# Kernel optimization log

Measured on AMD Instinct MI355X. Metric: run time of the kernel, lower is better.

The kernel has to match this reference:

```python
import jax, jax.numpy as jnp
import numpy as np

N_HEAD, D_HEAD, D_MODEL, D_INNER, KSIZE = 16, 64, 1024, 4096, 3
LN_EPS = 1e-3  # keras LayerNormalization default epsilon


def _layernorm(x, g, b):
    m = jnp.mean(x, axis=-1, keepdims=True)
    v = jnp.var(x, axis=-1, keepdims=True)
    return (x - m) * jax.lax.rsqrt(v + LN_EPS) * g + b


def _conv1d_same(x, w, b):
    # x: [B, S, Cin], w: [K, Cin, Cout] (keras Conv1D layout)
    y = jax.lax.conv_general_dilated(x, w, window_strides=(1,), padding='SAME',
                                     dimension_numbers=('NWC', 'WIO', 'NWC'))
    return y + b


def setup_inputs() -> dict:
    key = jax.random.key(0)
    ks = jax.random.split(key, 12)
    B, S, D = 4, 1024, D_MODEL
    dec_inp = jax.random.normal(ks[0], (B, S, D), dtype=jnp.float32)
    # padding mask: True = valid token; ensure >=1 padded position per row
    lengths = jax.random.randint(ks[1], (B,), S // 2, S)
    mask = (jnp.arange(S)[None, :] < lengths[:, None])[:, :, None]  # [B,S,1] bool
    sd = 0.02
    qkv_w = jax.random.normal(ks[2], (D, 3 * N_HEAD * D_HEAD), dtype=jnp.float32) * sd
    qkv_b = jnp.zeros((3 * N_HEAD * D_HEAD,), dtype=jnp.float32)
    o_w = jax.random.normal(ks[3], (N_HEAD * D_HEAD, D), dtype=jnp.float32) * sd
    ln1_g = jnp.ones((D,), dtype=jnp.float32)
    ln1_b = jnp.zeros((D,), dtype=jnp.float32)
    conv1_w = jax.random.normal(ks[4], (KSIZE, D, D_INNER), dtype=jnp.float32) * sd
    conv1_b = jnp.zeros((D_INNER,), dtype=jnp.float32)
    conv2_w = jax.random.normal(ks[5], (KSIZE, D_INNER, D), dtype=jnp.float32) * sd
    conv2_b = jnp.zeros((D,), dtype=jnp.float32)
    ln2_g = jnp.ones((D,), dtype=jnp.float32)
    ln2_b = jnp.zeros((D,), dtype=jnp.float32)
    return dict(dec_inp=dec_inp, mask=mask, qkv_w=qkv_w, qkv_b=qkv_b, o_w=o_w,
                ln1_g=ln1_g, ln1_b=ln1_b, conv1_w=conv1_w, conv1_b=conv1_b,
                conv2_w=conv2_w, conv2_b=conv2_b, ln2_g=ln2_g, ln2_b=ln2_b)


def _forward(dec_inp, mask, qkv_w, qkv_b, o_w, ln1_g, ln1_b,
             conv1_w, conv1_b, conv2_w, conv2_b, ln2_g, ln2_b):
    B, S, D = dec_inp.shape
    H, dh = N_HEAD, D_HEAD
    scale = 1.0 / (dh ** 0.5)
    # --- MultiHeadAttn (post-lnorm; dropout inactive at inference) ---
    residual = dec_inp
    qkv = dec_inp @ qkv_w + qkv_b                       # [B,S,3*H*dh]
    hq, hk, hv = jnp.split(qkv, 3, axis=2)
    to_flat = lambda h: h.reshape(B, S, H, dh).transpose(0, 2, 1, 3).reshape(B * H, S, dh)
    q, k, v = to_flat(hq), to_flat(hk), to_flat(hv)
    score = jnp.einsum('bqd,bkd->bqk', q, k) * scale    # [B*H, S, S]
    # attn_mask = ~mask.squeeze(2): True at PAD positions (faithful to TF port)
    am = (~mask[:, :, 0]).astype(score.dtype)[:, None, :]    # [B,1,S]
    am = jnp.tile(am, (H, S, 1))                             # [B*H,S,S] (tile over batch axis, as in tf.tile)
    add = jnp.where(am.astype(bool), am, -jnp.inf)           # pad -> +1.0, valid -> -inf (as written in source)
    score = score + add
    prob = jax.nn.softmax(score, axis=2)
    vec = prob @ v                                      # [B*H,S,dh]
    # faithful to source reshapes: [B*H,S,dh] -> [H,B,S,dh] -> [B,S,H*dh]
    vec = vec.reshape(H, B, S, dh).transpose(1, 2, 0, 3).reshape(B, S, H * dh)
    attn_out = vec @ o_w
    out = _layernorm(residual + attn_out, ln1_g, ln1_b)
    # mask-multiply between blocks
    out = out * mask.astype(out.dtype)
    # --- PositionwiseConvFF (post-lnorm) ---
    core = _conv1d_same(out, conv1_w, conv1_b)
    core = jax.nn.relu(core)
    core = _conv1d_same(core, conv2_w, conv2_b)
    out = _layernorm(out + core, ln2_g, ln2_b)
    out = out * mask.astype(out.dtype)
    return out


def reference(dec_inp, mask, qkv_w, qkv_b, o_w, ln1_g, ln1_b,
              conv1_w, conv1_b, conv2_w, conv2_b, ln2_g, ln2_b):
    return _forward(dec_inp, mask, qkv_w, qkv_b, o_w, ln1_g, ln1_b,
                    conv1_w, conv1_b, conv2_w, conv2_b, ln2_g, ln2_b)
```

## Files before the change

kernel.cpp:

```cpp
#include <hip/hip_runtime.h>
#include <cstdint>
#include <cstddef>

typedef float f32x4 __attribute__((ext_vector_type(4)));
typedef __bf16 bf16x8 __attribute__((ext_vector_type(8)));
typedef unsigned short u16;

__device__ __forceinline__ float bf2f(u16 u) {
  union { unsigned int i; float f; } x; x.i = ((unsigned int)u) << 16; return x.f;
}
__device__ __forceinline__ u16 f2bf(float f) {
  union { float f; unsigned int i; } x; x.f = f;
  unsigned int i = x.i;
  i += 0x7fffu + ((i >> 16) & 1u);
  return (u16)(i >> 16);
}

#if defined(__has_builtin)
#if __has_builtin(__builtin_amdgcn_global_load_lds)
#define HAS_GLL 1
#endif
#endif

__device__ __forceinline__ void async16(const u16* g, u16* l) {
#ifdef HAS_GLL
  __builtin_amdgcn_global_load_lds((const __attribute__((address_space(1))) void*)(const void*)g,
                                   (__attribute__((address_space(3))) void*)(void*)l, 16, 0, 0);
#else
  *(uint4*)l = *(const uint4*)g;
#endif
}

__global__ void compact_mask(const unsigned char* __restrict__ mask,
                             int* __restrict__ padIdx, int* __restrict__ padCnt,
                             float* __restrict__ maskf) {
  const int b = blockIdx.x;
  const int lane = threadIdx.x;
  int stride = 1;
  if (mask[1] == 0) stride = (mask[4] != 0) ? 4 : 8;
  int cnt = 0;
  for (int s0 = 0; s0 < 1024; s0 += 64) {
    const int s = s0 + lane;
    const bool valid = (mask[(size_t)((b << 10) + s) * stride] != 0);
    maskf[(b << 10) + s] = valid ? 1.f : 0.f;
    const bool pad = !valid;
    const unsigned long long bal = __ballot(pad);
    const int rank = (int)__popcll(bal & ((1ull << lane) - 1ull));
    if (pad) padIdx[(b << 10) + cnt + rank] = s;
    cnt += (int)__popcll(bal);
  }
  if (lane == 0) padCnt[b] = cnt;
}

__global__ __launch_bounds__(256)
void f32_to_bf16(const float* __restrict__ in, u16* __restrict__ out, int n4) {
  const int i = blockIdx.x * 256 + threadIdx.x;
  if (i < n4) {
    const float4 v = ((const float4*)in)[i];
    u16 o[4] = { f2bf(v.x), f2bf(v.y), f2bf(v.z), f2bf(v.w) };
    ((ushort4*)out)[i] = *(const ushort4*)o;
  }
}

__global__ __launch_bounds__(256)
void transpose_f32_bf16(const float* __restrict__ in, u16* __restrict__ out, int R, int C) {
  __shared__ u16 tile[64][65];
  const int r0 = blockIdx.y << 6, c0 = blockIdx.x << 6;
  const int tid = threadIdx.x;
  const int lr = tid >> 3, lc = (tid & 7) << 3;
#pragma unroll
  for (int p = 0; p < 2; ++p) {
    const int row = lr + (p << 5);
    const float4 a = *(const float4*)(in + (size_t)(r0 + row) * C + c0 + lc);
    const float4 bq = *(const float4*)(in + (size_t)(r0 + row) * C + c0 + lc + 4);
    tile[row][lc + 0] = f2bf(a.x); tile[row][lc + 1] = f2bf(a.y);
    tile[row][lc + 2] = f2bf(a.z); tile[row][lc + 3] = f2bf(a.w);
    tile[row][lc + 4] = f2bf(bq.x); tile[row][lc + 5] = f2bf(bq.y);
    tile[row][lc + 6] = f2bf(bq.z); tile[row][lc + 7] = f2bf(bq.w);
  }
  __syncthreads();
#pragma unroll
  for (int p = 0; p < 2; ++p) {
    const int oc = lr + (p << 5);
    u16 tmp[8];
#pragma unroll
    for (int e = 0; e < 8; ++e) tmp[e] = tile[lc + e][oc];
    *(uint4*)(out + (size_t)(c0 + oc) * R + r0 + lc) = *(const uint4*)tmp;
  }
}

template<int NTAPS, bool RELU, int SPLITK, int KORIG, int NBN>
__global__ __launch_bounds__(256)
void gemm_bt(const u16* __restrict__ A, const u16* __restrict__ BT,
             const float* __restrict__ bias, u16* __restrict__ C, u16* __restrict__ Calt,
             int M, int N, const u16* __restrict__ zp) {
  __shared__ __align__(16) u16 As[128 * 64];
  __shared__ __align__(16) u16 Bs[128 * 64];
  const int tid = threadIdx.x;
  const int id = blockIdx.x + NBN * blockIdx.y;
  const int bm = ((id / (16 * NBN)) << 4) + (id & 15);
  const int bn = (id % (16 * NBN)) >> 4;
  const int m0 = bm << 7;
  const int n0 = bn << 7;
  const int kz = (SPLITK > 1) ? blockIdx.z : 0;
  constexpr int Ktot = NTAPS * KORIG;
  constexpr int kchunk = Ktot / SPLITK;
  const int lane = tid & 63;
  const int w = tid >> 6;
  const int wm = (w >> 1) << 6;
  const int wn = (w & 1) << 6;
  const int fr = lane & 15;
  const int quad = lane >> 4;
  const int srow = tid >> 3;
  const int scol = (tid & 7) << 3;
  const int sx = (((tid & 7) ^ (srow & 7)) << 3);

  f32x4 acc[4][4] = {};

  const int kbeg = kz * kchunk, kend = kbeg + kchunk;
  int k = kbeg;
  while (k < kend) {
    const int t = (NTAPS == 3) ? (k / KORIG) : 0;
    const int seg_end = (NTAPS == 3) ? min(kend, (t + 1) * KORIG) : kend;
    const int c0 = k - t * KORIG;
    const u16* aptr[4];
    const u16* bptr[4];
#pragma unroll
    for (int i = 0; i < 4; ++i) {
      const int row = srow + (i << 5);
      if (NTAPS == 3) {
        const int m = m0 + row;
        const int sp = (m & 1023) + t - 1;
        aptr[i] = ((unsigned)sp < 1024u) ? (A + (size_t)(m + t - 1) * KORIG + c0 + sx)
                                         : (zp + ((tid & 255) << 3));
      } else {
        aptr[i] = A + (size_t)(m0 + row) * KORIG + k + sx;
      }
      bptr[i] = BT + (size_t)(n0 + row) * Ktot + k + sx;
    }
    for (; k < seg_end; k += 64) {
#pragma unroll
      for (int i = 0; i < 4; ++i) {
        const int row = srow + (i << 5);
        async16(aptr[i], &As[(row << 6) + scol]);
        async16(bptr[i], &Bs[(row << 6) + scol]);
        aptr[i] += 64; bptr[i] += 64;
      }
      asm volatile("s_waitcnt vmcnt(0)" ::: "memory");
      __syncthreads();
#pragma unroll
      for (int ks = 0; ks < 64; ks += 32) {
        const int ccol = ((((ks >> 3) + quad) ^ (fr & 7)) << 3);
        bf16x8 af[4], bfr[4];
#pragma unroll
        for (int mi = 0; mi < 4; ++mi)
          af[mi] = *(const bf16x8*)&As[((wm + (mi << 4) + fr) << 6) + ccol];
#pragma unroll
        for (int ni = 0; ni < 4; ++ni)
          bfr[ni] = *(const bf16x8*)&Bs[((wn + (ni << 4) + fr) << 6) + ccol];
#pragma unroll
        for (int mi = 0; mi < 4; ++mi)
#pragma unroll
          for (int ni = 0; ni < 4; ++ni)
            acc[mi][ni] = __builtin_amdgcn_mfma_f32_16x16x32_bf16(af[mi], bfr[ni], acc[mi][ni], 0, 0, 0);
      }
      __syncthreads();
    }
  }
  const int rbase = m0 + wm + (quad << 2);
  const int cbase = n0 + wn + fr;
  u16* dst = C;
  if (SPLITK > 1 && kz > 0) dst = Calt + (size_t)(kz - 1) * ((size_t)M * N);
#pragma unroll
  for (int ni = 0; ni < 4; ++ni) {
    const int col = cbase + (ni << 4);
    const float bv = (SPLITK == 1 && bias) ? bias[col] : 0.f;
#pragma unroll
    for (int mi = 0; mi < 4; ++mi) {
#pragma unroll
      for (int r = 0; r < 4; ++r) {
        float v = acc[mi][ni][r] + bv;
        if (RELU) v = fmaxf(v, 0.f);
        dst[(size_t)(rbase + (mi << 4) + r) * N + col] = f2bf(v);
      }
    }
  }
}

#define BAR8() do { asm volatile("" ::: "memory"); __builtin_amdgcn_s_barrier(); asm volatile("" ::: "memory"); } while (0)
#define WAITV(N) asm volatile("s_waitcnt vmcnt(" #N ")" ::: "memory")

#define READ_A(SLOT) \
  _Pragma("unroll") for (int mi = 0; mi < 4; ++mi) \
  _Pragma("unroll") for (int ks = 0; ks < 2; ++ks) \
    af[mi][ks] = *(const bf16x8*)&As[SLOT][((wm + (mi << 4) + fr) << 6) + ((((ks << 2) + quad) ^ (fr & 7)) << 3)];
#define READ_B(SLOT, BFR) \
  _Pragma("unroll") for (int ni = 0; ni < 2; ++ni) \
  _Pragma("unroll") for (int ks = 0; ks < 2; ++ks) \
    BFR[ni][ks] = *(const bf16x8*)&Bs[SLOT][((wn + (ni << 4) + fr) << 6) + ((((ks << 2) + quad) ^ (fr & 7)) << 3)];
#define MFMA_PH(MH, NH, BFR) \
  __builtin_amdgcn_s_setprio(1); \
  _Pragma("unroll") for (int mi = 0; mi < 4; ++mi) \
  _Pragma("unroll") for (int ni = 0; ni < 2; ++ni) \
  _Pragma("unroll") for (int ks = 0; ks < 2; ++ks) \
    acc[MH][mi][NH][ni] = __builtin_amdgcn_mfma_f32_16x16x32_bf16(af[mi][ks], BFR[ni][ks], acc[MH][mi][NH][ni], 0, 0, 0); \
  __builtin_amdgcn_s_setprio(0)

template<int NTAPS, bool RELU, int SPLITK, int KORIG>
__global__ __launch_bounds__(512, 2)
void gemm8(const u16* __restrict__ A, const u16* __restrict__ BT,
           const float* __restrict__ bias, u16* __restrict__ C, u16* __restrict__ Calt,
           int M, int N, const u16* __restrict__ zp) {
  __shared__ __align__(16) u16 As[4][128 * 64];
  __shared__ __align__(16) u16 Bs[4][128 * 64];
  constexpr int Ktot = NTAPS * KORIG;
  constexpr int kchunk = Ktot / SPLITK;
  constexpr int NT = kchunk / 64;
  const int tid = threadIdx.x;
  const int id = blockIdx.x;
  const int bm = id & 15, bn = id >> 4;
  const int m0 = bm << 8, n0 = bn << 8;
  const int kz = (SPLITK > 1) ? blockIdx.z : 0;
  const int kbeg = kz * kchunk;
  const int lane = tid & 63, w = tid >> 6;
  const int wm = (w >> 2) << 6;
  const int wn = (w & 3) << 5;
  const int fr = lane & 15, quad = lane >> 4;
  const int srow = tid >> 3;
  const int scol = (tid & 7) << 3;
  const int sx = (((tid & 7) ^ (srow & 7)) << 3);

  const u16* bp[2][2];
#pragma unroll
  for (int nh = 0; nh < 2; ++nh)
#pragma unroll
    for (int j = 0; j < 2; ++j)
      bp[nh][j] = BT + (size_t)(n0 + (nh << 7) + srow + (j << 6)) * Ktot + kbeg + sx;

  auto stageA = [&](int ts, int mh) {
    const int k = kbeg + (ts << 6);
    const int tap = (NTAPS == 3) ? (k / KORIG) : 0;
    const int c0 = k - tap * KORIG;
    u16* dst = &As[((ts & 1) << 1) | mh][(srow << 6) + scol];
    const int mrow = m0 + (mh << 7) + srow;
#pragma unroll
    for (int j = 0; j < 2; ++j) {
      const int m = mrow + (j << 6);
      const u16* src;
      if (NTAPS == 1) {
        src = A + (size_t)m * KORIG + c0 + sx;
      } else {
        const int sp = (m & 1023) + tap - 1;
        src = ((unsigned)sp < 1024u) ? (A + (size_t)(m + tap - 1) * KORIG + c0 + sx)
                                     : (zp + ((tid & 255) << 3));
      }
      async16(src, dst + (j << 12));
    }
  };
  auto stageB = [&](int ts, int nh) {
    u16* dst = &Bs[((ts & 1) << 1) | nh][(srow << 6) + scol];
#pragma unroll
    for (int j = 0; j < 2; ++j) {
      async16(bp[nh][j], dst + (j << 12));
      bp[nh][j] += 64;
    }
  };

  f32x4 acc[2][4][2][2] = {};
  bf16x8 af[4][2], bf0[2][2], bf1[2][2];

  stageA(0, 0); stageB(0, 0); stageB(0, 1); stageA(0, 1);
  WAITV(4);
  BAR8();

#pragma unroll 2
  for (int t = 0; t < NT; ++t) {
    const int s0 = (t & 1) << 1, s1 = s0 | 1;
    const bool pf = (t + 1 < NT);
    if (pf) stageA(t + 1, 0);
    READ_A(s0);
    READ_B(s0, bf0);
    BAR8();
    MFMA_PH(0, 0, bf0);
    if (pf) { WAITV(4); } else { WAITV(2); }
    BAR8();
    if (pf) stageB(t + 1, 0);
    READ_B(s1, bf1);
    BAR8();
    MFMA_PH(0, 1, bf1);
    if (pf) { WAITV(4); } else { WAITV(0); }
    BAR8();
    if (pf) stageB(t + 1, 1);
    READ_A(s1);
    BAR8();
    MFMA_PH(1, 1, bf1);
    BAR8();
    if (pf) stageA(t + 1, 1);
    BAR8();
    MFMA_PH(1, 0, bf0);
    if (pf) { WAITV(4); }
    BAR8();
  }

  u16* dst = C;
  if (SPLITK > 1 && kz > 0) dst = Calt + (size_t)(kz - 1) * ((size_t)M * N);
#pragma unroll
  for (int mh = 0; mh < 2; ++mh)
#pragma unroll
    for (int nh = 0; nh < 2; ++nh)
#pragma unroll
      for (int ni = 0; ni < 2; ++ni) {
        const int col = n0 + (nh << 7) + wn + (ni << 4) + fr;
        const float bv = (SPLITK == 1 && bias) ? bias[col] : 0.f;
#pragma unroll
        for (int mi = 0; mi < 4; ++mi)
#pragma unroll
          for (int r = 0; r < 4; ++r) {
            float v = acc[mh][mi][nh][ni][r] + bv;
            if (RELU) v = fmaxf(v, 0.f);
            dst[(size_t)(m0 + (mh << 7) + wm + (mi << 4) + (quad << 2) + r) * N + col] = f2bf(v);
          }
      }
}

__global__ __launch_bounds__(256)
void gather_v(const u16* __restrict__ qkv, const int* __restrict__ padIdx,
              const int* __restrict__ padCnt, u16* __restrict__ Vt) {
  const int bm = blockIdx.x;
  const int jt = blockIdx.y;
  const int b = bm >> 2, mb = bm & 3;
  const int npad = padCnt[mb];
  const int npadR = (npad + 63) & ~63;
  if (jt * 64 >= npadR) return;
  const int tid = threadIdx.x;
  __shared__ int rows[64];
  if (tid < 64) {
    const int j = jt * 64 + tid;
    const int jj = j < npad ? j : npad - 1;
    rows[tid] = padIdx[(mb << 10) + jj];
  }
  __shared__ u16 tile[64][72];
  for (int c = 0; c < 16; ++c) {
    const int ch0 = c << 6;
    __syncthreads();
#pragma unroll
    for (int p = 0; p < 2; ++p) {
      const int r = (tid >> 3) + (p << 5);
      const int ch = (tid & 7) << 3;
      const uint4 v = *(const uint4*)(qkv + (size_t)((b << 10) + rows[r]) * 3072 + 2048 + ch0 + ch);
      const u16* us = (const u16*)&v;
#pragma unroll
      for (int e = 0; e < 8; ++e) tile[r][ch + e] = us[e];
    }
    __syncthreads();
#pragma unroll
    for (int p = 0; p < 2; ++p) {
      const int r = (tid >> 3) + (p << 5);
      const int jc = (tid & 7) << 3;
      u16 tmp[8];
#pragma unroll
      for (int e = 0; e < 8; ++e) tmp[e] = tile[jc + e][r];
      *(uint4*)(Vt + (size_t)((bm << 10) + ch0 + r) * 512 + jt * 64 + jc) = *(const uint4*)tmp;
    }
  }
}

__global__ __launch_bounds__(256)
void attn_mfma(const u16* __restrict__ qkv, const u16* __restrict__ Vt,
               const int* __restrict__ padIdx, const int* __restrict__ padCnt,
               u16* __restrict__ vecS) {
  __shared__ __align__(16) u16 Ks[64 * 64];
  __shared__ __align__(16) u16 Vts[64 * 64];
  __shared__ __align__(16) u16 Ps[4][32 * 88];
  __shared__ int rowsIdx[512];
  const int i = blockIdx.x;
  const int qt = blockIdx.y;
  const int b = i >> 4, h = i & 15;
  const int mb = h & 3, bm = (b << 2) + mb;
  const int h_out = i >> 2;
  const int npad = padCnt[mb];
  const int nkt = (npad + 63) >> 6;
  const int tid = threadIdx.x;
  const int w = tid >> 6, lane = tid & 63;
  const int fr = lane & 15, quad = lane >> 4, fko = quad << 3;
  const int srow = tid >> 3, scol = (tid & 7) << 3;
  const int sx = (((tid & 7) ^ (srow & 7)) << 3);

#pragma unroll
  for (int p = 0; p < 2; ++p) {
    const int j = (p << 8) + tid;
    const int jj = j < npad ? j : npad - 1;
    rowsIdx[j] = padIdx[(mb << 10) + jj];
  }

  const int qw = (qt << 7) + (w << 5);
  bf16x8 qf[2][2];
#pragma unroll
  for (int rt = 0; rt < 2; ++rt)
#pragma unroll
    for (int ks = 0; ks < 2; ++ks)
      qf[rt][ks] = *(const bf16x8*)(qkv + (size_t)((b << 10) + qw + (rt << 4) + fr) * 3072 +
                                    (h << 6) + (ks << 5) + fko);

  f32x4 O[2][4];
  float mrun[2][4], lrun[2][4];
#pragma unroll
  for (int rt = 0; rt < 2; ++rt)
#pragma unroll
    for (int r = 0; r < 4; ++r) {
      mrun[rt][r] = -1e30f; lrun[rt][r] = 0.f;
#pragma unroll
      for (int dt = 0; dt < 4; ++dt) O[rt][dt][r] = 0.f;
    }
  __syncthreads();

  for (int kt = 0; kt < nkt; ++kt) {
#pragma unroll
    for (int p = 0; p < 2; ++p) {
      const int r = srow + (p << 5);
      const int grow = rowsIdx[(kt << 6) + r];
      async16(qkv + (size_t)((b << 10) + grow) * 3072 + 1024 + (h << 6) + sx,
              &Ks[(r << 6) + scol]);
      async16(Vt + (size_t)((bm << 10) + (h << 6) + r) * 512 + (kt << 6) + sx,
              &Vts[(r << 6) + scol]);
    }
    asm volatile("s_waitcnt vmcnt(0)" ::: "memory");
    __syncthreads();

    f32x4 S[2][4];
#pragma unroll
    for (int rt = 0; rt < 2; ++rt)
#pragma unroll
      for (int nt = 0; nt < 4; ++nt)
#pragma unroll
        for (int r = 0; r < 4; ++r) S[rt][nt][r] = 0.f;
#pragma unroll
    for (int ks = 0; ks < 2; ++ks) {
      const int ccol = ((((ks << 2) + quad) ^ (fr & 7)) << 3);
      bf16x8 bfr[4];
#pragma unroll
      for (int nt = 0; nt < 4; ++nt)
        bfr[nt] = *(const bf16x8*)&Ks[(((nt << 4) + fr) << 6) + ccol];
#pragma unroll
      for (int rt = 0; rt < 2; ++rt)
#pragma unroll
        for (int nt = 0; nt < 4; ++nt)
          S[rt][nt] = __builtin_amdgcn_mfma_f32_16x16x32_bf16(qf[rt][ks], bfr[nt], S[rt][nt], 0, 0, 0);
    }

#pragma unroll
    for (int nt = 0; nt < 4; ++nt) {
      const int key = (kt << 6) + (nt << 4) + fr;
      const bool dead = (key >= npad);
#pragma unroll
      for (int rt = 0; rt < 2; ++rt)
#pragma unroll
        for (int r = 0; r < 4; ++r) {
          float s = S[rt][nt][r] * 0.125f;
          S[rt][nt][r] = dead ? -1e30f : s;
        }
    }

#pragma unroll
    for (int rt = 0; rt < 2; ++rt) {
#pragma unroll
      for (int r = 0; r < 4; ++r) {
        float mx = fmaxf(fmaxf(S[rt][0][r], S[rt][1][r]), fmaxf(S[rt][2][r], S[rt][3][r]));
#pragma unroll
        for (int off = 1; off <= 8; off <<= 1) mx = fmaxf(mx, __shfl_xor(mx, off, 64));
        const float mnew = fmaxf(mrun[rt][r], mx);
        const float alpha = __expf(mrun[rt][r] - mnew);
        mrun[rt][r] = mnew;
        float rsum = 0.f;
#pragma unroll
        for (int nt = 0; nt < 4; ++nt) {
          const float p_ = __expf(S[rt][nt][r] - mnew);
          S[rt][nt][r] = p_;
          rsum += p_;
        }
#pragma unroll
        for (int off = 1; off <= 8; off <<= 1) rsum += __shfl_xor(rsum, off, 64);
        lrun[rt][r] = lrun[rt][r] * alpha + rsum;
#pragma unroll
        for (int dt = 0; dt < 4; ++dt) O[rt][dt][r] *= alpha;
      }
    }

    u16* ps = &Ps[w][0];
#pragma unroll
    for (int rt = 0; rt < 2; ++rt)
#pragma unroll
      for (int nt = 0; nt < 4; ++nt)
#pragma unroll
        for (int r = 0; r < 4; ++r)
          ps[((rt << 4) + (quad << 2) + r) * 88 + (nt << 4) + fr] = f2bf(S[rt][nt][r]);
    asm volatile("s_waitcnt lgkmcnt(0)" ::: "memory");

#pragma unroll
    for (int ks = 0; ks < 2; ++ks) {
      const int ccol = ((((ks << 2) + quad) ^ (fr & 7)) << 3);
      bf16x8 af[2], bv[4];
#pragma unroll
      for (int rt = 0; rt < 2; ++rt)
        af[rt] = *(const bf16x8*)&ps[((rt << 4) + fr) * 88 + (ks << 5) + fko];
#pragma unroll
      for (int dt = 0; dt < 4; ++dt)
        bv[dt] = *(const bf16x8*)&Vts[(((dt << 4) + fr) << 6) + ccol];
#pragma unroll
      for (int rt = 0; rt < 2; ++rt)
#pragma unroll
        for (int dt = 0; dt < 4; ++dt)
          O[rt][dt] = __builtin_amdgcn_mfma_f32_16x16x32_bf16(af[rt], bv[dt], O[rt][dt], 0, 0, 0);
    }
    __syncthreads();
  }

#pragma unroll
  for (int rt = 0; rt < 2; ++rt)
#pragma unroll
    for (int r = 0; r < 4; ++r) {
      const float inv = 1.f / lrun[rt][r];
      const int q = qw + (rt << 4) + (quad << 2) + r;
      u16* orow = vecS + (size_t)((mb << 10) + q) * 1024 + (h_out << 6);
#pragma unroll
      for (int dt = 0; dt < 4; ++dt)
        orow[(dt << 4) + fr] = f2bf(O[rt][dt][r] * inv);
    }
}

template<bool XF32, bool OUTF32, bool HASB>
__global__ __launch_bounds__(256)
void ln_red4(const void* __restrict__ Xv, const u16* __restrict__ P0,
             const u16* __restrict__ P1, int MN,
             const float* __restrict__ bias,
             const float* __restrict__ g, const float* __restrict__ be,
             const float* __restrict__ maskf, void* __restrict__ outv) {
  const int r = blockIdx.x;
  const int tid = threadIdx.x;
  const size_t base = (size_t)r << 10;
  const float* Xf = (const float*)Xv;
  const u16* Xb = (const u16*)Xv;
  float x[4];
  float s1 = 0.f, s2 = 0.f;
#pragma unroll
  for (int j = 0; j < 4; ++j) {
    const int c = (tid << 2) + j;
    const size_t idx = base + c;
    float y = bf2f(P0[idx]) + bf2f(P1[idx]) + bf2f(P1[MN + idx]) + bf2f(P1[2 * (size_t)MN + idx]);
    if (HASB) y += bias[c];
    const float xv = XF32 ? Xf[idx] : bf2f(Xb[idx]);
    const float v = xv + y;
    x[j] = v; s1 += v; s2 += v * v;
  }
#pragma unroll
  for (int off = 32; off > 0; off >>= 1) { s1 += __shfl_xor(s1, off, 64); s2 += __shfl_xor(s2, off, 64); }
  __shared__ float rs1[4], rs2[4];
  if ((tid & 63) == 0) { rs1[tid >> 6] = s1; rs2[tid >> 6] = s2; }
  __syncthreads();
  s1 = rs1[0] + rs1[1] + rs1[2] + rs1[3];
  s2 = rs2[0] + rs2[1] + rs2[2] + rs2[3];
  const float mean = s1 * (1.f / 1024.f);
  const float var = s2 * (1.f / 1024.f) - mean * mean;
  const float rstd = rsqrtf(var + 1e-3f);
  const float mv = maskf[r];
#pragma unroll
  for (int j = 0; j < 4; ++j) {
    const int c = (tid << 2) + j;
    const float y = ((x[j] - mean) * rstd * g[c] + be[c]) * mv;
    if (OUTF32) ((float*)outv)[base + c] = y;
    else ((u16*)outv)[base + c] = f2bf(y);
  }
}

extern "C" void kernel_launch(void* const* d_in, const int* in_sizes, int n_in,
                              void* d_out, int out_size, void* d_ws, size_t ws_size,
                              hipStream_t stream) {
  (void)in_sizes; (void)n_in; (void)out_size; (void)ws_size;
  const float* dec  = (const float*)d_in[0];
  const unsigned char* mask = (const unsigned char*)d_in[1];
  const float* wqkv = (const float*)d_in[2];
  const float* bqkv = (const float*)d_in[3];
  const float* wo   = (const float*)d_in[4];
  const float* g1   = (const float*)d_in[5];
  const float* b1   = (const float*)d_in[6];
  const float* w1   = (const float*)d_in[7];
  const float* bc1  = (const float*)d_in[8];
  const float* w2   = (const float*)d_in[9];
  const float* bc2  = (const float*)d_in[10];
  const float* g2   = (const float*)d_in[11];
  const float* b2   = (const float*)d_in[12];
  char* ws = (char*)d_ws;
  u16*   zp    = (u16*)(ws + 0);
  int*   pcnt  = (int*)(ws + 16384);
  float* maskf = (float*)(ws + 20480);
  int*   pidx  = (int*)(ws + 40960);
  u16*   decB  = (u16*)(ws + 65536);
  u16*   wqkvT = (u16*)(ws + 8454144);
  u16*   woT   = (u16*)(ws + 14745600);
  u16*   w1T   = (u16*)(ws + 16842752);
  u16*   w2T   = (u16*)(ws + 42008576);
  u16*   qkv   = (u16*)(ws + 67174400);
  u16*   Vt    = (u16*)(ws + 92340224);
  u16*   vecS  = (u16*)(ws + 109117440);
  u16*   x1bf  = (u16*)(ws + 8454144);
  u16*   ybuf  = (u16*)(ws + 67174400);
  u16*   aP0   = (u16*)(ws + 65536);
  u16*   aP1   = (u16*)(ws + 67174400);
  u16*   cP0   = (u16*)(ws + 65536);
  u16*   cP1   = (u16*)(ws + 16842752);

  hipMemsetAsync(zp, 0, 16384, stream);
  compact_mask<<<dim3(4), dim3(64), 0, stream>>>(mask, pidx, pcnt, maskf);
  f32_to_bf16<<<dim3(4096), dim3(256), 0, stream>>>(dec, decB, 1048576);
  transpose_f32_bf16<<<dim3(48, 16), dim3(256), 0, stream>>>(wqkv, wqkvT, 1024, 3072);
  transpose_f32_bf16<<<dim3(16, 16), dim3(256), 0, stream>>>(wo, woT, 1024, 1024);
  transpose_f32_bf16<<<dim3(64, 48), dim3(256), 0, stream>>>(w1, w1T, 3072, 4096);
  transpose_f32_bf16<<<dim3(16, 192), dim3(256), 0, stream>>>(w2, w2T, 12288, 1024);
  gemm8<1, false, 1, 1024><<<dim3(192), dim3(512), 0, stream>>>(decB, wqkvT, bqkv, qkv, nullptr, 4096, 3072, zp);
  gather_v<<<dim3(16, 8), dim3(256), 0, stream>>>(qkv, pidx, pcnt, Vt);
  attn_mfma<<<dim3(64, 8), dim3(256), 0, stream>>>(qkv, Vt, pidx, pcnt, vecS);
  gemm_bt<1, false, 4, 1024, 8><<<dim3(8, 32, 4), dim3(256), 0, stream>>>(vecS, woT, nullptr, aP0, aP1, 4096, 1024, zp);
  ln_red4<true, false, false><<<dim3(4096), dim3(256), 0, stream>>>(dec, aP0, aP1, 4194304, nullptr, g1, b1, maskf, x1bf);
  gemm8<3, true, 1, 1024><<<dim3(256), dim3(512), 0, stream>>>(x1bf, w1T, bc1, ybuf, nullptr, 4096, 4096, zp);
  gemm8<3, false, 4, 4096><<<dim3(64, 1, 4), dim3(512), 0, stream>>>(ybuf, w2T, nullptr, cP0, cP1, 4096, 1024, zp);
  ln_red4<false, true, true><<<dim3(4096), dim3(256), 0, stream>>>(x1bf, cP0, cP1, 4194304, bc2, g2, b2, maskf, (float*)d_out);
}
```

Baseline: 506.7 us.

## Restructure GEMM main loop to register-prefetch fragments per k-slice

Reorganizes the gemm8 inner loop so all four async global-to-LDS stages for the next tile are issued at the start of each iteration. LDS fragment reads are split by k-subslice and double-buffered in registers (afC/afN, bfk), with explicit lgkmcnt waits and sched_barriers so reads overlap with MFMA phases. The aim is to hide LDS read latency behind MFMA work and cut redundant B-fragment reloads. In exchange it uses more VGPRs, which may pressure the 2-blocks-per-CU launch bound, and it waits on all global loads once per iteration, which shortens the global prefetch window.

```diff
diff --git a/kernel.cpp b/kernel.cpp
--- a/kernel.cpp
+++ b/kernel.cpp
@@ -189,21 +189,22 @@
 
 #define BAR8() do { asm volatile("" ::: "memory"); __builtin_amdgcn_s_barrier(); asm volatile("" ::: "memory"); } while (0)
 #define WAITV(N) asm volatile("s_waitcnt vmcnt(" #N ")" ::: "memory")
-
-#define READ_A(SLOT) \
+#define LGKM(N) asm volatile("s_waitcnt lgkmcnt(" #N ")" ::: "memory")
+#define SB0() __builtin_amdgcn_sched_barrier(0)
+
+#define READ_AF(DST, SLOT, KS) \
   _Pragma("unroll") for (int mi = 0; mi < 4; ++mi) \
-  _Pragma("unroll") for (int ks = 0; ks < 2; ++ks) \
-    af[mi][ks] = *(const bf16x8*)&As[SLOT][((wm + (mi << 4) + fr) << 6) + ((((ks << 2) + quad) ^ (fr & 7)) << 3)];
-#define READ_B(SLOT, BFR) \
+    DST[mi] = *(const bf16x8*)&As[SLOT][((wm + (mi << 4) + fr) << 6) + (((((KS) << 2) + quad) ^ (fr & 7)) << 3)];
+#define READ_BF(KS, SP) \
+  _Pragma("unroll") for (int nh = 0; nh < 2; ++nh) \
   _Pragma("unroll") for (int ni = 0; ni < 2; ++ni) \
-  _Pragma("unroll") for (int ks = 0; ks < 2; ++ks) \
-    BFR[ni][ks] = *(const bf16x8*)&Bs[SLOT][((wn + (ni << 4) + fr) << 6) + ((((ks << 2) + quad) ^ (fr & 7)) << 3)];
-#define MFMA_PH(MH, NH, BFR) \
+    bfk[KS][nh][ni] = *(const bf16x8*)&Bs[(SP) | nh][((wn + (ni << 4) + fr) << 6) + (((((KS) << 2) + quad) ^ (fr & 7)) << 3)];
+#define MFMA_P(MH, AF, KS) \
   __builtin_amdgcn_s_setprio(1); \
   _Pragma("unroll") for (int mi = 0; mi < 4; ++mi) \
+  _Pragma("unroll") for (int nh = 0; nh < 2; ++nh) \
   _Pragma("unroll") for (int ni = 0; ni < 2; ++ni) \
-  _Pragma("unroll") for (int ks = 0; ks < 2; ++ks) \
-    acc[MH][mi][NH][ni] = __builtin_amdgcn_mfma_f32_16x16x32_bf16(af[mi][ks], BFR[ni][ks], acc[MH][mi][NH][ni], 0, 0, 0); \
+    acc[MH][mi][nh][ni] = __builtin_amdgcn_mfma_f32_16x16x32_bf16(AF[mi], bfk[KS][nh][ni], acc[MH][mi][nh][ni], 0, 0, 0); \
   __builtin_amdgcn_s_setprio(0)
 
 template<int NTAPS, bool RELU, int SPLITK, int KORIG>
@@ -267,38 +268,39 @@
   };
 
   f32x4 acc[2][4][2][2] = {};
-  bf16x8 af[4][2], bf0[2][2], bf1[2][2];
+  bf16x8 afC[4], afN[4], bfk[2][2][2];
 
   stageA(0, 0); stageB(0, 0); stageB(0, 1); stageA(0, 1);
-  WAITV(4);
+  WAITV(0);
   BAR8();
+  READ_AF(afC, 0, 0);
+  READ_BF(0, 0);
 
 #pragma unroll 2
   for (int t = 0; t < NT; ++t) {
-    const int s0 = (t & 1) << 1, s1 = s0 | 1;
+    const int s = (t & 1) << 1;
     const bool pf = (t + 1 < NT);
-    if (pf) stageA(t + 1, 0);
-    READ_A(s0);
-    READ_B(s0, bf0);
+    if (pf) { stageA(t + 1, 0); stageB(t + 1, 0); stageB(t + 1, 1); stageA(t + 1, 1); }
+    READ_AF(afN, s | 0, 1);
+    READ_BF(1, s);
     BAR8();
-    MFMA_PH(0, 0, bf0);
-    if (pf) { WAITV(4); } else { WAITV(2); }
+    LGKM(8); SB0();
+    MFMA_P(0, afC, 0);
+    READ_AF(afC, s | 1, 0);
     BAR8();
-    if (pf) stageB(t + 1, 0);
-    READ_B(s1, bf1);
+    LGKM(4); SB0();
+    MFMA_P(0, afN, 1);
+    READ_AF(afN, s | 1, 1);
     BAR8();
-    MFMA_PH(0, 1, bf1);
-    if (pf) { WAITV(4); } else { WAITV(0); }
+    LGKM(4); SB0();
+    MFMA_P(1, afC, 0);
+    WAITV(0);
     BAR8();
-    if (pf) stageB(t + 1, 1);
-    READ_A(s1);
+    if (pf) { READ_AF(afC, (s ^ 2) | 0, 0); READ_BF(0, s ^ 2); }
     BAR8();
-    MFMA_PH(1, 1, bf1);
-    BAR8();
-    if (pf) stageA(t + 1, 1);
-    BAR8();
-    MFMA_PH(1, 0, bf0);
-    if (pf) { WAITV(4); }
+    if (pf) { LGKM(8); } else { LGKM(0); }
+    SB0();
+    MFMA_P(1, afN, 1);
     BAR8();
   }
 
```

After: 659.9 us. 30.2% more time.

## Deepen GEMM global-to-LDS prefetch to two tiles and drop redundant barriers

Applied to the files above, without the earlier changes.

Reworks the GEMM main loop so async global-to-LDS loads are issued two K-tiles ahead instead of one. Each LDS slot is refilled right after all waves have pulled its fragments into registers, which is enforced by an explicit lgkmcnt(0) wait and a barrier. This cuts the barriers per iteration from eight to four and leaves more time to hide global-memory latency. In exchange there are more loads in flight, and correctness now depends on the new wait counts and slot reuse being exactly right.

```diff
diff --git a/kernel.cpp b/kernel.cpp
--- a/kernel.cpp
+++ b/kernel.cpp
@@ -189,6 +189,7 @@
 
 #define BAR8() do { asm volatile("" ::: "memory"); __builtin_amdgcn_s_barrier(); asm volatile("" ::: "memory"); } while (0)
 #define WAITV(N) asm volatile("s_waitcnt vmcnt(" #N ")" ::: "memory")
+#define LGKM0() asm volatile("s_waitcnt lgkmcnt(0)" ::: "memory")
 
 #define READ_A(SLOT) \
   _Pragma("unroll") for (int mi = 0; mi < 4; ++mi) \
@@ -270,36 +271,36 @@
   bf16x8 af[4][2], bf0[2][2], bf1[2][2];
 
   stageA(0, 0); stageB(0, 0); stageB(0, 1); stageA(0, 1);
-  WAITV(4);
+  if (NT > 1) {
+    stageA(1, 0); stageB(1, 0); stageB(1, 1); stageA(1, 1);
+    WAITV(8);
+  } else {
+    WAITV(0);
+  }
   BAR8();
 
 #pragma unroll 2
   for (int t = 0; t < NT; ++t) {
-    const int s0 = (t & 1) << 1, s1 = s0 | 1;
-    const bool pf = (t + 1 < NT);
-    if (pf) stageA(t + 1, 0);
-    READ_A(s0);
-    READ_B(s0, bf0);
+    const int s = (t & 1) << 1;
+    const bool pf2 = (t + 2 < NT);
+    READ_A(s | 0);
+    READ_B(s | 0, bf0);
+    LGKM0();
     BAR8();
     MFMA_PH(0, 0, bf0);
-    if (pf) { WAITV(4); } else { WAITV(2); }
-    BAR8();
-    if (pf) stageB(t + 1, 0);
-    READ_B(s1, bf1);
+    if (pf2) { stageA(t + 2, 0); stageB(t + 2, 0); }
+    READ_B(s | 1, bf1);
+    LGKM0();
     BAR8();
     MFMA_PH(0, 1, bf1);
-    if (pf) { WAITV(4); } else { WAITV(0); }
-    BAR8();
-    if (pf) stageB(t + 1, 1);
-    READ_A(s1);
+    if (pf2) stageB(t + 2, 1);
+    READ_A(s | 1);
+    LGKM0();
     BAR8();
     MFMA_PH(1, 1, bf1);
-    BAR8();
-    if (pf) stageA(t + 1, 1);
+    if (pf2) { stageA(t + 2, 1); WAITV(8); } else { WAITV(0); }
     BAR8();
     MFMA_PH(1, 0, bf0);
-    if (pf) { WAITV(4); }
-    BAR8();
   }
 
   u16* dst = C;
```

Measured after the change: 476.4 us. -6.0%, faster.
